# Performance work log

Hardware: AMD Instinct MI355X
Metric: run time of the kernel (lower is better)

## Reference

```python
import jax, jax.numpy as jnp
import numpy as np

D = 1024
K = 8
EPS_BN = 1e-5
EPS_L2 = 1e-8


def l2norm(x, axis=-1):
    return x / (jnp.sqrt(jnp.sum(x * x, axis=axis, keepdims=True)) + EPS_L2)


def setup_inputs() -> dict:
    key = jax.random.key(0)
    ks = jax.random.split(key, 12)
    B, T = 256, 72
    H = D // K
    s1 = 1.0 / np.sqrt(D)
    s2 = 1.0 / np.sqrt(H)
    return {
        "img_embed": jax.random.normal(ks[0], (B, 36, D), dtype=jnp.float32),
        "cap_embed": jax.random.normal(ks[1], (B, T, D), dtype=jnp.float32),
        "lens": jax.random.randint(ks[2], (B,), 1, T + 1),
        # fc_gamma: Linear(D,H) -> ReLU -> Linear(H,D); weights stored (in,out)
        "Wg1": jax.random.uniform(ks[3], (D, H), jnp.float32, -s1, s1),
        "bg1": jax.random.uniform(ks[4], (H,), jnp.float32, -s1, s1),
        "Wg2": jax.random.uniform(ks[5], (H, D), jnp.float32, -s2, s2),
        "bg2": jax.random.uniform(ks[6], (D,), jnp.float32, -s2, s2),
        # fc_beta
        "Wb1": jax.random.uniform(ks[7], (D, H), jnp.float32, -s1, s1),
        "bb1": jax.random.uniform(ks[8], (H,), jnp.float32, -s1, s1),
        "Wb2": jax.random.uniform(ks[9], (H, D), jnp.float32, -s2, s2),
        "bb2": jax.random.uniform(ks[10], (D,), jnp.float32, -s2, s2),
    }


def reference(img_embed, cap_embed, lens, Wg1, bg1, Wg2, bg2, Wb1, bb1, Wb2, bb2):
    # img_embed: (B, 36, D), cap_embed: (B, T, D), lens: (B,)
    B, T, _ = cap_embed.shape

    # img_repr: mean over 36 regions -> (B, D)
    img_repr = img_embed.mean(axis=1)

    # BatchNorm1d (affine=False, training): stats over (batch, time) per feature.
    # cap in torch is (B, D, T); stats reduce over batch+time axes.
    mean = cap_embed.mean(axis=(0, 1))                      # (D,)
    var = jnp.mean((cap_embed - mean) ** 2, axis=(0, 1))    # biased, (D,)
    norm_feat = (cap_embed - mean) / jnp.sqrt(var + EPS_BN)  # (B, T, D)

    # Masked mean pooling over valid timesteps (BN stats precede masking,
    # matching the original). Pooling is linear, so conditional affine
    # (gamma,beta constant over time) commutes with it.
    mask = (jnp.arange(T)[None, :] < lens[:, None]).astype(cap_embed.dtype)  # (B, T)
    pooled = jnp.einsum('btd,bt->bd', norm_feat, mask) / lens[:, None].astype(cap_embed.dtype)  # (B_cap, D)

    # Conditional gamma/beta per image
    gammas = jax.nn.relu(img_repr @ Wg1 + bg1) @ Wg2 + bg2   # (B_img, D)
    betas = jax.nn.relu(img_repr @ Wb1 + bb1) @ Wb2 + bb2    # (B_img, D)

    # txt[i, j, :] = pooled[j] * (gamma_i + 1) + beta_i
    txt = pooled[None, :, :] * (gammas[:, None, :] + 1.0) + betas[:, None, :]  # (B_img, B_cap, D)
    txt_n = l2norm(txt, axis=-1)
    img_n = l2norm(img_repr, axis=-1)                        # (B_img, D)

    # sim for image i over captions j; original writes sims[:, i] = sim
    sim_ij = jnp.einsum('id,ijd->ij', img_n, txt_n)          # (B_img, B_cap)
    return sim_ij.T                                          # sims[j, i]
```

## Files before the change

kernel.cpp:

```cpp
#include <hip/hip_runtime.h>
#include <math.h>

#define NDIM 1024
#define HDIM 128
#define NB 256
#define NT 72
#define NR 36

__device__ __forceinline__ float wave_sum(float v) {
#pragma unroll
  for (int off = 32; off > 0; off >>= 1) v += __shfl_down(v, off, 64);
  return v;
}

__device__ __forceinline__ float dot4(const float4 a, const float4 b) {
  return a.x * b.x + a.y * b.y + a.z * b.z + a.w * b.w;
}

__global__ __launch_bounds__(256) void k_cap1(const float* __restrict__ cap,
                                              const int* __restrict__ lens,
                                              float* __restrict__ fs, float* __restrict__ fq,
                                              float* __restrict__ ms) {
  const int b = blockIdx.x & 255;
  const int half = blockIdx.x >> 8;
  const int tid = threadIdx.x;
  const int len = lens[b];
  const int t0 = half * 36;
  const float* base = cap + (size_t)b * NT * NDIM + (size_t)t0 * NDIM + tid * 4;
  float fsx = 0.f, fsy = 0.f, fsz = 0.f, fsw = 0.f;
  float fqx = 0.f, fqy = 0.f, fqz = 0.f, fqw = 0.f;
  float msx = 0.f, msy = 0.f, msz = 0.f, msw = 0.f;
#pragma unroll 12
  for (int tt = 0; tt < 36; ++tt) {
    const float4 v = *reinterpret_cast<const float4*>(base + tt * NDIM);
    fsx += v.x; fsy += v.y; fsz += v.z; fsw += v.w;
    fqx += v.x * v.x; fqy += v.y * v.y; fqz += v.z * v.z; fqw += v.w * v.w;
    if (t0 + tt < len) { msx += v.x; msy += v.y; msz += v.z; msw += v.w; }
  }
  const int o = (half * NB + b) * NDIM + tid * 4;
  *reinterpret_cast<float4*>(fs + o) = make_float4(fsx, fsy, fsz, fsw);
  *reinterpret_cast<float4*>(fq + o) = make_float4(fqx, fqy, fqz, fqw);
  *reinterpret_cast<float4*>(ms + o) = make_float4(msx, msy, msz, msw);
}

__global__ __launch_bounds__(256) void k_stats(const float* __restrict__ fs,
                                               const float* __restrict__ fq,
                                               float* __restrict__ meanv,
                                               float* __restrict__ rstdv) {
  const int dloc = threadIdx.x & 63;
  const int grp = threadIdx.x >> 6;
  const int d = blockIdx.x * 64 + dloc;
  float s = 0.f, q = 0.f;
  const int r0 = grp * 128;
#pragma unroll 8
  for (int r = r0; r < r0 + 128; ++r) {
    s += fs[r * NDIM + d];
    q += fq[r * NDIM + d];
  }
  __shared__ float ss[4][64], sq2[4][64];
  ss[grp][dloc] = s;
  sq2[grp][dloc] = q;
  __syncthreads();
  if (threadIdx.x < 64) {
    s = ss[0][dloc] + ss[1][dloc] + ss[2][dloc] + ss[3][dloc];
    q = sq2[0][dloc] + sq2[1][dloc] + sq2[2][dloc] + sq2[3][dloc];
    const float invN = 1.0f / (float)(NB * NT);
    const float m = s * invN;
    const float var = q * invN - m * m;
    meanv[d] = m;
    rstdv[d] = 1.0f / sqrtf(var + 1e-5f);
  }
}

__global__ __launch_bounds__(256) void k_pool(const float* __restrict__ ms,
                                              const int* __restrict__ lens,
                                              const float* __restrict__ meanv,
                                              const float* __restrict__ rstdv,
                                              float* __restrict__ pooled, float* __restrict__ p2) {
  const int b = blockIdx.x, tid = threadIdx.x;
  const float invl = 1.0f / (float)lens[b];
  const int d = tid * 4;
  const float4 m0 = *reinterpret_cast<const float4*>(ms + (size_t)b * NDIM + d);
  const float4 m1 = *reinterpret_cast<const float4*>(ms + (size_t)(NB + b) * NDIM + d);
  const float4 mu = *reinterpret_cast<const float4*>(meanv + d);
  const float4 rs = *reinterpret_cast<const float4*>(rstdv + d);
  const float px = ((m0.x + m1.x) * invl - mu.x) * rs.x;
  const float py = ((m0.y + m1.y) * invl - mu.y) * rs.y;
  const float pz = ((m0.z + m1.z) * invl - mu.z) * rs.z;
  const float pw = ((m0.w + m1.w) * invl - mu.w) * rs.w;
  *reinterpret_cast<float4*>(pooled + b * NDIM + d) = make_float4(px, py, pz, pw);
  *reinterpret_cast<float4*>(p2 + b * NDIM + d) = make_float4(px * px, py * py, pz * pz, pw * pw);
}

__global__ __launch_bounds__(1024) void k_imgmean(const float* __restrict__ img,
                                                  float* __restrict__ repr,
                                                  float* __restrict__ imgn) {
  const int b = blockIdx.x, tid = threadIdx.x;
  const int col = tid & 255;
  const int rg = tid >> 8;
  __shared__ float4 part[4][256];
  __shared__ float red[4];
  __shared__ float sInv;
  const float* base = img + (size_t)b * NR * NDIM + (size_t)rg * 9 * NDIM + col * 4;
  float sx = 0.f, sy = 0.f, sz = 0.f, sw = 0.f;
#pragma unroll
  for (int r = 0; r < 9; ++r) {
    const float4 v = *reinterpret_cast<const float4*>(base + r * NDIM);
    sx += v.x; sy += v.y; sz += v.z; sw += v.w;
  }
  part[rg][col] = make_float4(sx, sy, sz, sw);
  __syncthreads();
  float mx = 0.f, my = 0.f, mz = 0.f, mw = 0.f;
  if (tid < 256) {
    const float4 a = part[0][tid], b4 = part[1][tid], c = part[2][tid], d4 = part[3][tid];
    const float inv = 1.0f / (float)NR;
    mx = (a.x + b4.x + c.x + d4.x) * inv;
    my = (a.y + b4.y + c.y + d4.y) * inv;
    mz = (a.z + b4.z + c.z + d4.z) * inv;
    mw = (a.w + b4.w + c.w + d4.w) * inv;
    *reinterpret_cast<float4*>(repr + (size_t)b * NDIM + tid * 4) = make_float4(mx, my, mz, mw);
    const float sq = wave_sum(mx * mx + my * my + mz * mz + mw * mw);
    if ((tid & 63) == 0) red[tid >> 6] = sq;
  }
  __syncthreads();
  if (tid == 0) sInv = 1.0f / (sqrtf(red[0] + red[1] + red[2] + red[3]) + 1e-8f);
  __syncthreads();
  if (tid < 256) {
    const float iv = sInv;
    *reinterpret_cast<float4*>(imgn + (size_t)b * NDIM + tid * 4) =
        make_float4(mx * iv, my * iv, mz * iv, mw * iv);
  }
}

__global__ __launch_bounds__(512) void k_l1(const float* __restrict__ repr,
                                            const float* __restrict__ Wg1,
                                            const float* __restrict__ Wb1,
                                            float* __restrict__ hpart) {
  const int g = blockIdx.x, br = blockIdx.y, ks = blockIdx.z;
  const int b0 = g * 8;
  const int kbase = ks * 128;
  const int tid = threadIdx.x;
  const int h2 = tid & 63;
  const int ksub = tid >> 6;
  const float* __restrict__ W = br ? Wb1 : Wg1;
  __shared__ float shr[8][128];
  __shared__ float sacc[8][128][8];
  {
    const int im = tid >> 6, c2 = (tid & 63) * 2;
    *reinterpret_cast<float2*>(&shr[im][c2]) =
        *reinterpret_cast<const float2*>(repr + (size_t)(b0 + im) * NDIM + kbase + c2);
  }
  __syncthreads();
  float acc0[8] = {0, 0, 0, 0, 0, 0, 0, 0}, acc1[8] = {0, 0, 0, 0, 0, 0, 0, 0};
#pragma unroll
  for (int q = 0; q < 4; ++q) {
    const int dl = ksub * 16 + q * 4;
    const float* wq = W + (size_t)(kbase + dl) * HDIM + h2;
    const float wa0 = wq[0], wa1 = wq[128], wa2 = wq[256], wa3 = wq[384];
    const float wb0 = wq[64], wb1 = wq[192], wb2 = wq[320], wb3 = wq[448];
#pragma unroll
    for (int i = 0; i < 8; ++i) {
      const float4 s = *reinterpret_cast<const float4*>(&shr[i][dl]);
      acc0[i] += s.x * wa0 + s.y * wa1 + s.z * wa2 + s.w * wa3;
      acc1[i] += s.x * wb0 + s.y * wb1 + s.z * wb2 + s.w * wb3;
    }
  }
#pragma unroll
  for (int i = 0; i < 8; ++i) {
    sacc[ksub][h2][i] = acc0[i];
    sacc[ksub][h2 + 64][i] = acc1[i];
  }
  __syncthreads();
#pragma unroll
  for (int v = tid; v < 1024; v += 512) {
    const int hh = v & 127, im = v >> 7;
    float s = 0.f;
#pragma unroll
    for (int k2 = 0; k2 < 8; ++k2) s += sacc[k2][hh][im];
    hpart[(((size_t)ks * 2 + br) * NB + b0 + im) * HDIM + hh] = s;
  }
}

__global__ __launch_bounds__(512) void k_l2(
    const float* __restrict__ hpart, const float* __restrict__ bg1,
    const float* __restrict__ bb1, const float* __restrict__ Wg2,
    const float* __restrict__ bg2, const float* __restrict__ Wb2,
    const float* __restrict__ bb2, const float* __restrict__ imgn, float* __restrict__ uarr,
    float* __restrict__ aarr, float* __restrict__ bvarr, float* __restrict__ cpart,
    float* __restrict__ epart) {
  const int gb = blockIdx.x, dgrp = blockIdx.y;
  const int b0 = gb * 4;
  const int tid = threadIdx.x;
  const int dl = tid & 127;
  const int d = dgrp * 128 + dl;
  const int ig = tid >> 7;
  __shared__ float shh[2][4][HDIM];
  __shared__ float sred[8][2];
#pragma unroll
  for (int v = tid; v < 1024; v += 512) {
    const int brv = v >> 9, rem = v & 511, im = rem >> 7, hh = rem & 127;
    float s = 0.f;
#pragma unroll
    for (int k2 = 0; k2 < 8; ++k2)
      s += hpart[(((size_t)k2 * 2 + brv) * NB + b0 + im) * HDIM + hh];
    s += brv ? bb1[hh] : bg1[hh];
    shh[brv][im][hh] = fmaxf(s, 0.f);
  }
  __syncthreads();
  float ga = 0.f, ba = 0.f;
#pragma unroll 8
  for (int q = 0; q < 32; ++q) {
    const int h = q * 4;
    const float4 hg = *reinterpret_cast<const float4*>(&shh[0][ig][h]);
    const float4 hb = *reinterpret_cast<const float4*>(&shh[1][ig][h]);
    const float* wgp = Wg2 + (size_t)h * NDIM + d;
    const float* wbp = Wb2 + (size_t)h * NDIM + d;
    ga += hg.x * wgp[0] + hg.y * wgp[1024] + hg.z * wgp[2048] + hg.w * wgp[3072];
    ba += hb.x * wbp[0] + hb.y * wbp[1024] + hb.z * wbp[2048] + hb.w * wbp[3072];
  }
  const float ox = ga + bg2[d] + 1.0f;
  const float tb = ba + bb2[d];
  const size_t o = (size_t)(b0 + ig) * NDIM + d;
  const float nv = imgn[o];
  uarr[o] = nv * ox;
  aarr[o] = ox * ox;
  bvarr[o] = ox * tb;
  const float c = wave_sum(nv * tb);
  const float e = wave_sum(tb * tb);
  const int lane = tid & 63, wv = tid >> 6;
  if (lane == 0) { sred[wv][0] = c; sred[wv][1] = e; }
  __syncthreads();
  if (tid < 8) {
    const int im = tid >> 1, isE = tid & 1;
    const float vv = sred[im * 2][isE] + sred[im * 2 + 1][isE];
    (isE ? epart : cpart)[dgrp * NB + b0 + im] = vv;
  }
}

#define DC 32
__global__ __launch_bounds__(256) void k_simtile(
    const float* __restrict__ uarr, const float* __restrict__ aarr,
    const float* __restrict__ bvarr, const float* __restrict__ pooled,
    const float* __restrict__ p2, float* __restrict__ pn, float* __restrict__ pa,
    float* __restrict__ pb) {
  __shared__ float su[32][36], sa[32][36], sb[32][36], sp[32][36], sq[32][36];
  const int tid = threadIdx.x;
  const int tx = tid & 15, ty = tid >> 4;
  const int i0 = blockIdx.x * 32, j0 = blockIdx.y * 32;
  const int k0 = blockIdx.z * 256;
  const int lr = tid >> 3;
  const int lc = (tid & 7) * 4;
  float an00 = 0, an01 = 0, an10 = 0, an11 = 0;
  float aa00 = 0, aa01 = 0, aa10 = 0, aa11 = 0;
  float ab00 = 0, ab01 = 0, ab10 = 0, ab11 = 0;
  for (int dc = k0; dc < k0 + 256; dc += DC) {
    __syncthreads();
    *reinterpret_cast<float4*>(&su[lr][lc]) =
        *reinterpret_cast<const float4*>(uarr + (i0 + lr) * NDIM + dc + lc);
    *reinterpret_cast<float4*>(&sa[lr][lc]) =
        *reinterpret_cast<const float4*>(aarr + (i0 + lr) * NDIM + dc + lc);
    *reinterpret_cast<float4*>(&sb[lr][lc]) =
        *reinterpret_cast<const float4*>(bvarr + (i0 + lr) * NDIM + dc + lc);
    *reinterpret_cast<float4*>(&sp[lr][lc]) =
        *reinterpret_cast<const float4*>(pooled + (j0 + lr) * NDIM + dc + lc);
    *reinterpret_cast<float4*>(&sq[lr][lc]) =
        *reinterpret_cast<const float4*>(p2 + (j0 + lr) * NDIM + dc + lc);
    __syncthreads();
#pragma unroll
    for (int dd = 0; dd < DC; dd += 4) {
      const float4 ru0 = *reinterpret_cast<const float4*>(&su[tx][dd]);
      const float4 ru1 = *reinterpret_cast<const float4*>(&su[tx + 16][dd]);
      const float4 ra0 = *reinterpret_cast<const float4*>(&sa[tx][dd]);
      const float4 ra1 = *reinterpret_cast<const float4*>(&sa[tx + 16][dd]);
      const float4 rb0 = *reinterpret_cast<const float4*>(&sb[tx][dd]);
      const float4 rb1 = *reinterpret_cast<const float4*>(&sb[tx + 16][dd]);
      const float4 rp0 = *reinterpret_cast<const float4*>(&sp[ty][dd]);
      const float4 rp1 = *reinterpret_cast<const float4*>(&sp[ty + 16][dd]);
      const float4 rq0 = *reinterpret_cast<const float4*>(&sq[ty][dd]);
      const float4 rq1 = *reinterpret_cast<const float4*>(&sq[ty + 16][dd]);
      an00 += dot4(ru0, rp0); an01 += dot4(ru0, rp1);
      an10 += dot4(ru1, rp0); an11 += dot4(ru1, rp1);
      aa00 += dot4(ra0, rq0); aa01 += dot4(ra0, rq1);
      aa10 += dot4(ra1, rq0); aa11 += dot4(ra1, rq1);
      ab00 += dot4(rb0, rp0); ab01 += dot4(rb0, rp1);
      ab10 += dot4(rb1, rp0); ab11 += dot4(rb1, rp1);
    }
  }
  const int s = blockIdx.z;
  const int i = i0 + tx, j = j0 + ty;
  size_t o = ((size_t)s * 256 + j) * 256 + i;
  pn[o] = an00; pa[o] = aa00; pb[o] = ab00;
  o = ((size_t)s * 256 + (j + 16)) * 256 + i;
  pn[o] = an01; pa[o] = aa01; pb[o] = ab01;
  o = ((size_t)s * 256 + j) * 256 + (i + 16);
  pn[o] = an10; pa[o] = aa10; pb[o] = ab10;
  o = ((size_t)s * 256 + (j + 16)) * 256 + (i + 16);
  pn[o] = an11; pa[o] = aa11; pb[o] = ab11;
}

__global__ __launch_bounds__(256) void k_reduce(const float* __restrict__ pn,
                                                const float* __restrict__ pa,
                                                const float* __restrict__ pb,
                                                const float* __restrict__ cpart,
                                                const float* __restrict__ epart,
                                                float* __restrict__ out) {
  const int j = blockIdx.x, i = threadIdx.x;
  const size_t base = (size_t)j * 256 + i;
  float n = 0.f, a = 0.f, b2 = 0.f;
#pragma unroll
  for (int s = 0; s < 4; ++s) {
    const size_t o = base + (size_t)s * 65536;
    n += pn[o]; a += pa[o]; b2 += pb[o];
  }
  float cv = 0.f, ev = 0.f;
#pragma unroll
  for (int s = 0; s < 8; ++s) { cv += cpart[s * NB + i]; ev += epart[s * NB + i]; }
  const float num = n + cv;
  const float den2 = a + 2.0f * b2 + ev;
  out[base] = num / (sqrtf(fmaxf(den2, 0.0f)) + 1e-8f);
}

extern "C" void kernel_launch(void* const* d_in, const int* in_sizes, int n_in,
                              void* d_out, int out_size, void* d_ws, size_t ws_size,
                              hipStream_t stream) {
  const float* img = (const float*)d_in[0];
  const float* cap = (const float*)d_in[1];
  const int* lens = (const int*)d_in[2];
  const float* Wg1 = (const float*)d_in[3];
  const float* bg1 = (const float*)d_in[4];
  const float* Wg2 = (const float*)d_in[5];
  const float* bg2 = (const float*)d_in[6];
  const float* Wb1 = (const float*)d_in[7];
  const float* bb1 = (const float*)d_in[8];
  const float* Wb2 = (const float*)d_in[9];
  const float* bb2 = (const float*)d_in[10];
  float* out = (float*)d_out;

  float* w = (float*)d_ws;
  float* fullsum = w; w += 2 * NB * NDIM;
  float* fullsq = w;  w += 2 * NB * NDIM;
  float* msum = w;    w += 2 * NB * NDIM;
  float* pooled = w;  w += NB * NDIM;
  float* p2 = w;      w += NB * NDIM;
  float* uarr = w;    w += NB * NDIM;
  float* aarr = w;    w += NB * NDIM;
  float* bvarr = w;   w += NB * NDIM;
  float* meanv = w;   w += NDIM;
  float* rstdv = w;   w += NDIM;
  float* cpart = w;   w += 8 * NB;
  float* epart = w;   w += 8 * NB;
  float* repr = fullsum;
  float* imgn = fullsum + NB * NDIM;
  float* hpart = msum;
  float* pn = fullsq;
  float* pa = fullsq + NB * NDIM;
  float* pb = fullsum;

  hipLaunchKernelGGL(k_cap1, dim3(512), dim3(256), 0, stream, cap, lens, fullsum, fullsq, msum);
  hipLaunchKernelGGL(k_stats, dim3(16), dim3(256), 0, stream, fullsum, fullsq, meanv, rstdv);
  hipLaunchKernelGGL(k_imgmean, dim3(NB), dim3(1024), 0, stream, img, repr, imgn);
  hipLaunchKernelGGL(k_pool, dim3(NB), dim3(256), 0, stream, msum, lens, meanv, rstdv, pooled, p2);
  hipLaunchKernelGGL(k_l1, dim3(32, 2, 8), dim3(512), 0, stream, repr, Wg1, Wb1, hpart);
  hipLaunchKernelGGL(k_l2, dim3(64, 8), dim3(512), 0, stream, hpart, bg1, bb1, Wg2, bg2, Wb2,
                     bb2, imgn, uarr, aarr, bvarr, cpart, epart);
  hipLaunchKernelGGL(k_simtile, dim3(8, 8, 4), dim3(256), 0, stream, uarr, aarr, bvarr, pooled,
                     p2, pn, pa, pb);
  hipLaunchKernelGGL(k_reduce, dim3(NB), dim3(256), 0, stream, pn, pa, pb, cpart, epart, out);
}
```

Baseline: 84.27 us.

## Fuse front-end kernels, retile similarity GEMM to 64x64 with finer K split

Caption statistics and image mean are merged into one launch, and BN stats, pooling and the first MLP layer into a second launch, with block-index dispatch choosing the role. This cuts the launch count from eight to five. The similarity tile grows to 64x64 per block with a 16-way K split. The squared pooled values are now computed in registers instead of read from a p2 buffer, and the a and 2b denominator terms are merged into one accumulator by pre-scaling bvarr by 2. The cost is more split-K partials for the reduce kernel to read, and workspace aliasing where the partial buffers spill over into adjacent arrays once those are no longer needed.

```diff
diff --git a/kernel.cpp b/kernel.cpp
--- a/kernel.cpp
+++ b/kernel.cpp
@@ -6,6 +6,7 @@
 #define NB 256
 #define NT 72
 #define NR 36
+#define KS 16
 
 __device__ __forceinline__ float wave_sum(float v) {
 #pragma unroll
@@ -17,167 +18,145 @@
   return a.x * b.x + a.y * b.y + a.z * b.z + a.w * b.w;
 }
 
-__global__ __launch_bounds__(256) void k_cap1(const float* __restrict__ cap,
-                                              const int* __restrict__ lens,
-                                              float* __restrict__ fs, float* __restrict__ fq,
-                                              float* __restrict__ ms) {
-  const int b = blockIdx.x & 255;
-  const int half = blockIdx.x >> 8;
-  const int tid = threadIdx.x;
-  const int len = lens[b];
-  const int t0 = half * 36;
-  const float* base = cap + (size_t)b * NT * NDIM + (size_t)t0 * NDIM + tid * 4;
-  float fsx = 0.f, fsy = 0.f, fsz = 0.f, fsw = 0.f;
-  float fqx = 0.f, fqy = 0.f, fqz = 0.f, fqw = 0.f;
-  float msx = 0.f, msy = 0.f, msz = 0.f, msw = 0.f;
-#pragma unroll 12
-  for (int tt = 0; tt < 36; ++tt) {
-    const float4 v = *reinterpret_cast<const float4*>(base + tt * NDIM);
-    fsx += v.x; fsy += v.y; fsz += v.z; fsw += v.w;
-    fqx += v.x * v.x; fqy += v.y * v.y; fqz += v.z * v.z; fqw += v.w * v.w;
-    if (t0 + tt < len) { msx += v.x; msy += v.y; msz += v.z; msw += v.w; }
-  }
-  const int o = (half * NB + b) * NDIM + tid * 4;
-  *reinterpret_cast<float4*>(fs + o) = make_float4(fsx, fsy, fsz, fsw);
-  *reinterpret_cast<float4*>(fq + o) = make_float4(fqx, fqy, fqz, fqw);
-  *reinterpret_cast<float4*>(ms + o) = make_float4(msx, msy, msz, msw);
-}
-
-__global__ __launch_bounds__(256) void k_stats(const float* __restrict__ fs,
-                                               const float* __restrict__ fq,
-                                               float* __restrict__ meanv,
-                                               float* __restrict__ rstdv) {
-  const int dloc = threadIdx.x & 63;
-  const int grp = threadIdx.x >> 6;
-  const int d = blockIdx.x * 64 + dloc;
-  float s = 0.f, q = 0.f;
-  const int r0 = grp * 128;
-#pragma unroll 8
-  for (int r = r0; r < r0 + 128; ++r) {
-    s += fs[r * NDIM + d];
-    q += fq[r * NDIM + d];
-  }
-  __shared__ float ss[4][64], sq2[4][64];
-  ss[grp][dloc] = s;
-  sq2[grp][dloc] = q;
-  __syncthreads();
-  if (threadIdx.x < 64) {
-    s = ss[0][dloc] + ss[1][dloc] + ss[2][dloc] + ss[3][dloc];
-    q = sq2[0][dloc] + sq2[1][dloc] + sq2[2][dloc] + sq2[3][dloc];
-    const float invN = 1.0f / (float)(NB * NT);
-    const float m = s * invN;
-    const float var = q * invN - m * m;
-    meanv[d] = m;
-    rstdv[d] = 1.0f / sqrtf(var + 1e-5f);
-  }
-}
-
-__global__ __launch_bounds__(256) void k_pool(const float* __restrict__ ms,
-                                              const int* __restrict__ lens,
-                                              const float* __restrict__ meanv,
-                                              const float* __restrict__ rstdv,
-                                              float* __restrict__ pooled, float* __restrict__ p2) {
-  const int b = blockIdx.x, tid = threadIdx.x;
-  const float invl = 1.0f / (float)lens[b];
-  const int d = tid * 4;
-  const float4 m0 = *reinterpret_cast<const float4*>(ms + (size_t)b * NDIM + d);
-  const float4 m1 = *reinterpret_cast<const float4*>(ms + (size_t)(NB + b) * NDIM + d);
-  const float4 mu = *reinterpret_cast<const float4*>(meanv + d);
-  const float4 rs = *reinterpret_cast<const float4*>(rstdv + d);
-  const float px = ((m0.x + m1.x) * invl - mu.x) * rs.x;
-  const float py = ((m0.y + m1.y) * invl - mu.y) * rs.y;
-  const float pz = ((m0.z + m1.z) * invl - mu.z) * rs.z;
-  const float pw = ((m0.w + m1.w) * invl - mu.w) * rs.w;
-  *reinterpret_cast<float4*>(pooled + b * NDIM + d) = make_float4(px, py, pz, pw);
-  *reinterpret_cast<float4*>(p2 + b * NDIM + d) = make_float4(px * px, py * py, pz * pz, pw * pw);
-}
-
-__global__ __launch_bounds__(1024) void k_imgmean(const float* __restrict__ img,
-                                                  float* __restrict__ repr,
-                                                  float* __restrict__ imgn) {
-  const int b = blockIdx.x, tid = threadIdx.x;
-  const int col = tid & 255;
-  const int rg = tid >> 8;
-  __shared__ float4 part[4][256];
+__global__ __launch_bounds__(256) void k_front(const float* __restrict__ img,
+                                               const float* __restrict__ cap,
+                                               const int* __restrict__ lens,
+                                               float* __restrict__ fs, float* __restrict__ fq,
+                                               float* __restrict__ ms, float* __restrict__ repr,
+                                               float* __restrict__ imgn) {
+  const int bid = blockIdx.x, tid = threadIdx.x;
   __shared__ float red[4];
   __shared__ float sInv;
-  const float* base = img + (size_t)b * NR * NDIM + (size_t)rg * 9 * NDIM + col * 4;
-  float sx = 0.f, sy = 0.f, sz = 0.f, sw = 0.f;
-#pragma unroll
-  for (int r = 0; r < 9; ++r) {
-    const float4 v = *reinterpret_cast<const float4*>(base + r * NDIM);
-    sx += v.x; sy += v.y; sz += v.z; sw += v.w;
-  }
-  part[rg][col] = make_float4(sx, sy, sz, sw);
-  __syncthreads();
-  float mx = 0.f, my = 0.f, mz = 0.f, mw = 0.f;
-  if (tid < 256) {
-    const float4 a = part[0][tid], b4 = part[1][tid], c = part[2][tid], d4 = part[3][tid];
+  if (bid < 512) {
+    const int b = bid & 255;
+    const int half = bid >> 8;
+    const int len = lens[b];
+    const int t0 = half * 36;
+    const float* base = cap + (size_t)b * NT * NDIM + (size_t)t0 * NDIM + tid * 4;
+    float fsx = 0.f, fsy = 0.f, fsz = 0.f, fsw = 0.f;
+    float fqx = 0.f, fqy = 0.f, fqz = 0.f, fqw = 0.f;
+    float msx = 0.f, msy = 0.f, msz = 0.f, msw = 0.f;
+#pragma unroll 12
+    for (int tt = 0; tt < 36; ++tt) {
+      const float4 v = *reinterpret_cast<const float4*>(base + tt * NDIM);
+      fsx += v.x; fsy += v.y; fsz += v.z; fsw += v.w;
+      fqx += v.x * v.x; fqy += v.y * v.y; fqz += v.z * v.z; fqw += v.w * v.w;
+      if (t0 + tt < len) { msx += v.x; msy += v.y; msz += v.z; msw += v.w; }
+    }
+    const int o = (half * NB + b) * NDIM + tid * 4;
+    *reinterpret_cast<float4*>(fs + o) = make_float4(fsx, fsy, fsz, fsw);
+    *reinterpret_cast<float4*>(fq + o) = make_float4(fqx, fqy, fqz, fqw);
+    *reinterpret_cast<float4*>(ms + o) = make_float4(msx, msy, msz, msw);
+  } else {
+    const int b = bid - 512;
+    const float* base = img + (size_t)b * NR * NDIM + tid * 4;
+    float sx = 0.f, sy = 0.f, sz = 0.f, sw = 0.f;
+#pragma unroll 12
+    for (int r = 0; r < NR; ++r) {
+      const float4 v = *reinterpret_cast<const float4*>(base + r * NDIM);
+      sx += v.x; sy += v.y; sz += v.z; sw += v.w;
+    }
     const float inv = 1.0f / (float)NR;
-    mx = (a.x + b4.x + c.x + d4.x) * inv;
-    my = (a.y + b4.y + c.y + d4.y) * inv;
-    mz = (a.z + b4.z + c.z + d4.z) * inv;
-    mw = (a.w + b4.w + c.w + d4.w) * inv;
-    *reinterpret_cast<float4*>(repr + (size_t)b * NDIM + tid * 4) = make_float4(mx, my, mz, mw);
-    const float sq = wave_sum(mx * mx + my * my + mz * mz + mw * mw);
-    if ((tid & 63) == 0) red[tid >> 6] = sq;
-  }
-  __syncthreads();
-  if (tid == 0) sInv = 1.0f / (sqrtf(red[0] + red[1] + red[2] + red[3]) + 1e-8f);
-  __syncthreads();
-  if (tid < 256) {
+    sx *= inv; sy *= inv; sz *= inv; sw *= inv;
+    *reinterpret_cast<float4*>(repr + (size_t)b * NDIM + tid * 4) = make_float4(sx, sy, sz, sw);
+    const float sq = wave_sum(sx * sx + sy * sy + sz * sz + sw * sw);
+    const int lane = tid & 63, wv = tid >> 6;
+    if (lane == 0) red[wv] = sq;
+    __syncthreads();
+    if (tid == 0) sInv = 1.0f / (sqrtf(red[0] + red[1] + red[2] + red[3]) + 1e-8f);
+    __syncthreads();
     const float iv = sInv;
     *reinterpret_cast<float4*>(imgn + (size_t)b * NDIM + tid * 4) =
-        make_float4(mx * iv, my * iv, mz * iv, mw * iv);
-  }
-}
-
-__global__ __launch_bounds__(512) void k_l1(const float* __restrict__ repr,
-                                            const float* __restrict__ Wg1,
-                                            const float* __restrict__ Wb1,
-                                            float* __restrict__ hpart) {
-  const int g = blockIdx.x, br = blockIdx.y, ks = blockIdx.z;
-  const int b0 = g * 8;
-  const int kbase = ks * 128;
-  const int tid = threadIdx.x;
-  const int h2 = tid & 63;
-  const int ksub = tid >> 6;
-  const float* __restrict__ W = br ? Wb1 : Wg1;
+        make_float4(sx * iv, sy * iv, sz * iv, sw * iv);
+  }
+}
+
+__global__ __launch_bounds__(512) void k_mid(const float* __restrict__ fs,
+                                             const float* __restrict__ fq,
+                                             const float* __restrict__ ms,
+                                             const int* __restrict__ lens,
+                                             const float* __restrict__ repr,
+                                             const float* __restrict__ Wg1,
+                                             const float* __restrict__ Wb1,
+                                             float* __restrict__ pooled,
+                                             float* __restrict__ hpart) {
+  const int bid = blockIdx.x, tid = threadIdx.x;
+  __shared__ float ss[8][64], sq2[8][64], smu[64], srs[64];
   __shared__ float shr[8][128];
   __shared__ float sacc[8][128][8];
-  {
-    const int im = tid >> 6, c2 = (tid & 63) * 2;
-    *reinterpret_cast<float2*>(&shr[im][c2]) =
-        *reinterpret_cast<const float2*>(repr + (size_t)(b0 + im) * NDIM + kbase + c2);
-  }
-  __syncthreads();
-  float acc0[8] = {0, 0, 0, 0, 0, 0, 0, 0}, acc1[8] = {0, 0, 0, 0, 0, 0, 0, 0};
-#pragma unroll
-  for (int q = 0; q < 4; ++q) {
-    const int dl = ksub * 16 + q * 4;
-    const float* wq = W + (size_t)(kbase + dl) * HDIM + h2;
-    const float wa0 = wq[0], wa1 = wq[128], wa2 = wq[256], wa3 = wq[384];
-    const float wb0 = wq[64], wb1 = wq[192], wb2 = wq[320], wb3 = wq[448];
+  if (bid < 16) {
+    const int d0 = bid * 64, dloc = tid & 63, grp = tid >> 6;
+    float s = 0.f, q = 0.f;
+    const int r0 = grp * 64;
+#pragma unroll 8
+    for (int r = r0; r < r0 + 64; ++r) {
+      s += fs[(size_t)r * NDIM + d0 + dloc];
+      q += fq[(size_t)r * NDIM + d0 + dloc];
+    }
+    ss[grp][dloc] = s;
+    sq2[grp][dloc] = q;
+    __syncthreads();
+    if (tid < 64) {
+      float S = 0.f, Q = 0.f;
+#pragma unroll
+      for (int g2 = 0; g2 < 8; ++g2) { S += ss[g2][tid]; Q += sq2[g2][tid]; }
+      const float invN = 1.0f / (float)(NB * NT);
+      const float mu = S * invN;
+      const float var = Q * invN - mu * mu;
+      smu[tid] = mu;
+      srs[tid] = 1.0f / sqrtf(var + 1e-5f);
+    }
+    __syncthreads();
+    const int dcol = tid & 63, brow = tid >> 6;
+    const float mu = smu[dcol], rs = srs[dcol];
+#pragma unroll 4
+    for (int b = brow; b < NB; b += 8) {
+      const float invl = 1.0f / (float)lens[b];
+      const float m = ms[(size_t)b * NDIM + d0 + dcol] + ms[(size_t)(NB + b) * NDIM + d0 + dcol];
+      pooled[(size_t)b * NDIM + d0 + dcol] = (m * invl - mu) * rs;
+    }
+  } else {
+    const int idx = bid - 16;
+    const int g = idx & 31, br = (idx >> 5) & 1, ks = idx >> 6;
+    const int b0 = g * 8;
+    const int kbase = ks * 128;
+    const int h2 = tid & 63;
+    const int ksub = tid >> 6;
+    const float* __restrict__ W = br ? Wb1 : Wg1;
+    {
+      const int im = tid >> 6, c2 = (tid & 63) * 2;
+      *reinterpret_cast<float2*>(&shr[im][c2]) =
+          *reinterpret_cast<const float2*>(repr + (size_t)(b0 + im) * NDIM + kbase + c2);
+    }
+    __syncthreads();
+    float acc0[8] = {0, 0, 0, 0, 0, 0, 0, 0}, acc1[8] = {0, 0, 0, 0, 0, 0, 0, 0};
+#pragma unroll
+    for (int q = 0; q < 4; ++q) {
+      const int dl = ksub * 16 + q * 4;
+      const float* wq = W + (size_t)(kbase + dl) * HDIM + h2;
+      const float wa0 = wq[0], wa1 = wq[128], wa2 = wq[256], wa3 = wq[384];
+      const float wb0 = wq[64], wb1 = wq[192], wb2 = wq[320], wb3 = wq[448];
+#pragma unroll
+      for (int i = 0; i < 8; ++i) {
+        const float4 s = *reinterpret_cast<const float4*>(&shr[i][dl]);
+        acc0[i] += s.x * wa0 + s.y * wa1 + s.z * wa2 + s.w * wa3;
+        acc1[i] += s.x * wb0 + s.y * wb1 + s.z * wb2 + s.w * wb3;
+      }
+    }
 #pragma unroll
     for (int i = 0; i < 8; ++i) {
-      const float4 s = *reinterpret_cast<const float4*>(&shr[i][dl]);
-      acc0[i] += s.x * wa0 + s.y * wa1 + s.z * wa2 + s.w * wa3;
-      acc1[i] += s.x * wb0 + s.y * wb1 + s.z * wb2 + s.w * wb3;
-    }
-  }
-#pragma unroll
-  for (int i = 0; i < 8; ++i) {
-    sacc[ksub][h2][i] = acc0[i];
-    sacc[ksub][h2 + 64][i] = acc1[i];
-  }
-  __syncthreads();
-#pragma unroll
-  for (int v = tid; v < 1024; v += 512) {
-    const int hh = v & 127, im = v >> 7;
-    float s = 0.f;
-#pragma unroll
-    for (int k2 = 0; k2 < 8; ++k2) s += sacc[k2][hh][im];
-    hpart[(((size_t)ks * 2 + br) * NB + b0 + im) * HDIM + hh] = s;
+      sacc[ksub][h2][i] = acc0[i];
+      sacc[ksub][h2 + 64][i] = acc1[i];
+    }
+    __syncthreads();
+#pragma unroll
+    for (int v = tid; v < 1024; v += 512) {
+      const int hh = v & 127, im = v >> 7;
+      float s = 0.f;
+#pragma unroll
+      for (int k2 = 0; k2 < 8; ++k2) s += sacc[k2][hh][im];
+      hpart[(((size_t)ks * 2 + br) * NB + b0 + im) * HDIM + hh] = s;
+    }
   }
 }
 
@@ -224,7 +203,7 @@
   const float nv = imgn[o];
   uarr[o] = nv * ox;
   aarr[o] = ox * ox;
-  bvarr[o] = ox * tb;
+  bvarr[o] = 2.0f * ox * tb;
   const float c = wave_sum(nv * tb);
   const float e = wave_sum(tb * tb);
   const int lane = tid & 63, wv = tid >> 6;
@@ -237,86 +216,87 @@
   }
 }
 
-#define DC 32
 __global__ __launch_bounds__(256) void k_simtile(
     const float* __restrict__ uarr, const float* __restrict__ aarr,
     const float* __restrict__ bvarr, const float* __restrict__ pooled,
-    const float* __restrict__ p2, float* __restrict__ pn, float* __restrict__ pa,
-    float* __restrict__ pb) {
-  __shared__ float su[32][36], sa[32][36], sb[32][36], sp[32][36], sq[32][36];
+    float* __restrict__ pn, float* __restrict__ pd) {
+  __shared__ float su[64][36], sa[64][36], sb[64][36], sp[64][36];
   const int tid = threadIdx.x;
   const int tx = tid & 15, ty = tid >> 4;
-  const int i0 = blockIdx.x * 32, j0 = blockIdx.y * 32;
-  const int k0 = blockIdx.z * 256;
+  const int i0 = blockIdx.x * 64, j0 = blockIdx.y * 64;
+  const int k0 = blockIdx.z * (NDIM / KS);
   const int lr = tid >> 3;
   const int lc = (tid & 7) * 4;
-  float an00 = 0, an01 = 0, an10 = 0, an11 = 0;
-  float aa00 = 0, aa01 = 0, aa10 = 0, aa11 = 0;
-  float ab00 = 0, ab01 = 0, ab10 = 0, ab11 = 0;
-  for (int dc = k0; dc < k0 + 256; dc += DC) {
-    __syncthreads();
-    *reinterpret_cast<float4*>(&su[lr][lc]) =
-        *reinterpret_cast<const float4*>(uarr + (i0 + lr) * NDIM + dc + lc);
-    *reinterpret_cast<float4*>(&sa[lr][lc]) =
-        *reinterpret_cast<const float4*>(aarr + (i0 + lr) * NDIM + dc + lc);
-    *reinterpret_cast<float4*>(&sb[lr][lc]) =
-        *reinterpret_cast<const float4*>(bvarr + (i0 + lr) * NDIM + dc + lc);
-    *reinterpret_cast<float4*>(&sp[lr][lc]) =
-        *reinterpret_cast<const float4*>(pooled + (j0 + lr) * NDIM + dc + lc);
-    *reinterpret_cast<float4*>(&sq[lr][lc]) =
-        *reinterpret_cast<const float4*>(p2 + (j0 + lr) * NDIM + dc + lc);
-    __syncthreads();
-#pragma unroll
-    for (int dd = 0; dd < DC; dd += 4) {
-      const float4 ru0 = *reinterpret_cast<const float4*>(&su[tx][dd]);
-      const float4 ru1 = *reinterpret_cast<const float4*>(&su[tx + 16][dd]);
-      const float4 ra0 = *reinterpret_cast<const float4*>(&sa[tx][dd]);
-      const float4 ra1 = *reinterpret_cast<const float4*>(&sa[tx + 16][dd]);
-      const float4 rb0 = *reinterpret_cast<const float4*>(&sb[tx][dd]);
-      const float4 rb1 = *reinterpret_cast<const float4*>(&sb[tx + 16][dd]);
-      const float4 rp0 = *reinterpret_cast<const float4*>(&sp[ty][dd]);
-      const float4 rp1 = *reinterpret_cast<const float4*>(&sp[ty + 16][dd]);
-      const float4 rq0 = *reinterpret_cast<const float4*>(&sq[ty][dd]);
-      const float4 rq1 = *reinterpret_cast<const float4*>(&sq[ty + 16][dd]);
-      an00 += dot4(ru0, rp0); an01 += dot4(ru0, rp1);
-      an10 += dot4(ru1, rp0); an11 += dot4(ru1, rp1);
-      aa00 += dot4(ra0, rq0); aa01 += dot4(ra0, rq1);
-      aa10 += dot4(ra1, rq0); aa11 += dot4(ra1, rq1);
-      ab00 += dot4(rb0, rp0); ab01 += dot4(rb0, rp1);
-      ab10 += dot4(rb1, rp0); ab11 += dot4(rb1, rp1);
+  float an[4][4] = {{0}}, ad[4][4] = {{0}};
+  for (int dc = k0; dc < k0 + NDIM / KS; dc += 32) {
+    __syncthreads();
+#pragma unroll
+    for (int rep = 0; rep < 2; ++rep) {
+      const int r = lr + rep * 32;
+      *reinterpret_cast<float4*>(&su[r][lc]) =
+          *reinterpret_cast<const float4*>(uarr + (size_t)(i0 + r) * NDIM + dc + lc);
+      *reinterpret_cast<float4*>(&sa[r][lc]) =
+          *reinterpret_cast<const float4*>(aarr + (size_t)(i0 + r) * NDIM + dc + lc);
+      *reinterpret_cast<float4*>(&sb[r][lc]) =
+          *reinterpret_cast<const float4*>(bvarr + (size_t)(i0 + r) * NDIM + dc + lc);
+      *reinterpret_cast<float4*>(&sp[r][lc]) =
+          *reinterpret_cast<const float4*>(pooled + (size_t)(j0 + r) * NDIM + dc + lc);
+    }
+    __syncthreads();
+#pragma unroll
+    for (int dd = 0; dd < 32; dd += 4) {
+      float4 rp[4], rq[4];
+#pragma unroll
+      for (int n = 0; n < 4; ++n) {
+        rp[n] = *reinterpret_cast<const float4*>(&sp[ty + 16 * n][dd]);
+        rq[n] = make_float4(rp[n].x * rp[n].x, rp[n].y * rp[n].y, rp[n].z * rp[n].z,
+                            rp[n].w * rp[n].w);
+      }
+#pragma unroll
+      for (int m = 0; m < 4; ++m) {
+        const float4 ru = *reinterpret_cast<const float4*>(&su[tx + 16 * m][dd]);
+        const float4 ra = *reinterpret_cast<const float4*>(&sa[tx + 16 * m][dd]);
+        const float4 rb = *reinterpret_cast<const float4*>(&sb[tx + 16 * m][dd]);
+#pragma unroll
+        for (int n = 0; n < 4; ++n) {
+          an[m][n] += dot4(ru, rp[n]);
+          ad[m][n] += dot4(ra, rq[n]) + dot4(rb, rp[n]);
+        }
+      }
     }
   }
   const int s = blockIdx.z;
-  const int i = i0 + tx, j = j0 + ty;
-  size_t o = ((size_t)s * 256 + j) * 256 + i;
-  pn[o] = an00; pa[o] = aa00; pb[o] = ab00;
-  o = ((size_t)s * 256 + (j + 16)) * 256 + i;
-  pn[o] = an01; pa[o] = aa01; pb[o] = ab01;
-  o = ((size_t)s * 256 + j) * 256 + (i + 16);
-  pn[o] = an10; pa[o] = aa10; pb[o] = ab10;
-  o = ((size_t)s * 256 + (j + 16)) * 256 + (i + 16);
-  pn[o] = an11; pa[o] = aa11; pb[o] = ab11;
+#pragma unroll
+  for (int m = 0; m < 4; ++m) {
+#pragma unroll
+    for (int n = 0; n < 4; ++n) {
+      const int i = i0 + tx + 16 * m, j = j0 + ty + 16 * n;
+      const size_t o = ((size_t)s * NB + j) * NB + i;
+      pn[o] = an[m][n];
+      pd[o] = ad[m][n];
+    }
+  }
 }
 
 __global__ __launch_bounds__(256) void k_reduce(const float* __restrict__ pn,
-                                                const float* __restrict__ pa,
-                                                const float* __restrict__ pb,
+                                                const float* __restrict__ pd,
                                                 const float* __restrict__ cpart,
                                                 const float* __restrict__ epart,
                                                 float* __restrict__ out) {
   const int j = blockIdx.x, i = threadIdx.x;
-  const size_t base = (size_t)j * 256 + i;
-  float n = 0.f, a = 0.f, b2 = 0.f;
-#pragma unroll
-  for (int s = 0; s < 4; ++s) {
-    const size_t o = base + (size_t)s * 65536;
-    n += pn[o]; a += pa[o]; b2 += pb[o];
+  const size_t base = (size_t)j * NB + i;
+  float n = 0.f, den = 0.f;
+#pragma unroll
+  for (int s = 0; s < KS; ++s) {
+    const size_t o = base + (size_t)s * (NB * NB);
+    n += pn[o];
+    den += pd[o];
   }
   float cv = 0.f, ev = 0.f;
 #pragma unroll
   for (int s = 0; s < 8; ++s) { cv += cpart[s * NB + i]; ev += epart[s * NB + i]; }
   const float num = n + cv;
-  const float den2 = a + 2.0f * b2 + ev;
+  const float den2 = den + ev;
   out[base] = num / (sqrtf(fmaxf(den2, 0.0f)) + 1e-8f);
 }
 
@@ -340,30 +320,25 @@
   float* fullsum = w; w += 2 * NB * NDIM;
   float* fullsq = w;  w += 2 * NB * NDIM;
   float* msum = w;    w += 2 * NB * NDIM;
+  float* hpart = w;   w += 16 * NB * HDIM;
   float* pooled = w;  w += NB * NDIM;
-  float* p2 = w;      w += NB * NDIM;
   float* uarr = w;    w += NB * NDIM;
   float* aarr = w;    w += NB * NDIM;
   float* bvarr = w;   w += NB * NDIM;
-  float* meanv = w;   w += NDIM;
-  float* rstdv = w;   w += NDIM;
   float* cpart = w;   w += 8 * NB;
   float* epart = w;   w += 8 * NB;
-  float* repr = fullsum;
-  float* imgn = fullsum + NB * NDIM;
-  float* hpart = msum;
-  float* pn = fullsq;
-  float* pa = fullsq + NB * NDIM;
-  float* pb = fullsum;
-
-  hipLaunchKernelGGL(k_cap1, dim3(512), dim3(256), 0, stream, cap, lens, fullsum, fullsq, msum);
-  hipLaunchKernelGGL(k_stats, dim3(16), dim3(256), 0, stream, fullsum, fullsq, meanv, rstdv);
-  hipLaunchKernelGGL(k_imgmean, dim3(NB), dim3(1024), 0, stream, img, repr, imgn);
-  hipLaunchKernelGGL(k_pool, dim3(NB), dim3(256), 0, stream, msum, lens, meanv, rstdv, pooled, p2);
-  hipLaunchKernelGGL(k_l1, dim3(32, 2, 8), dim3(512), 0, stream, repr, Wg1, Wb1, hpart);
+  float* repr = uarr;
+  float* imgn = aarr;
+  float* pn = fullsum;
+  float* pd = msum;
+
+  hipLaunchKernelGGL(k_front, dim3(768), dim3(256), 0, stream, img, cap, lens, fullsum, fullsq,
+                     msum, repr, imgn);
+  hipLaunchKernelGGL(k_mid, dim3(528), dim3(512), 0, stream, fullsum, fullsq, msum, lens, repr,
+                     Wg1, Wb1, pooled, hpart);
   hipLaunchKernelGGL(k_l2, dim3(64, 8), dim3(512), 0, stream, hpart, bg1, bb1, Wg2, bg2, Wb2,
                      bb2, imgn, uarr, aarr, bvarr, cpart, epart);
-  hipLaunchKernelGGL(k_simtile, dim3(8, 8, 4), dim3(256), 0, stream, uarr, aarr, bvarr, pooled,
-                     p2, pn, pa, pb);
-  hipLaunchKernelGGL(k_reduce, dim3(NB), dim3(256), 0, stream, pn, pa, pb, cpart, epart, out);
-}
+  hipLaunchKernelGGL(k_simtile, dim3(4, 4, KS), dim3(256), 0, stream, uarr, aarr, bvarr, pooled,
+                     pn, pd);
+  hipLaunchKernelGGL(k_reduce, dim3(NB), dim3(256), 0, stream, pn, pd, cpart, epart, out);
+}
```

After: 86.39 us. +2.5%, slower.
